# Performance work log

Hardware: AMD Instinct MI355X
Metric: run time of the kernel (lower is better)

Reference implementation:

```python
import jax, jax.numpy as jnp
import numpy as np

WS = 7
C = 384
NH = 12
HD = C // NH
HID = 4 * C


def layernorm(x, g, b, eps=1e-5):
    m = jnp.mean(x, axis=-1, keepdims=True)
    v = jnp.mean((x - m) ** 2, axis=-1, keepdims=True)
    return (x - m) * jax.lax.rsqrt(v + eps) * g + b


def setup_inputs() -> dict:
    key = jax.random.key(0)
    ks = jax.random.split(key, 12)
    s = 0.02
    return {
        "tokens": jax.random.normal(ks[0], (2, 8, 56 * 56, C), jnp.float32),
        "in_proj_w": jax.random.normal(ks[1], (3 * C, C), jnp.float32) * s,
        "in_proj_b": jnp.zeros((3 * C,), jnp.float32),
        "out_w": jax.random.normal(ks[2], (C, C), jnp.float32) * s,
        "out_b": jnp.zeros((C,), jnp.float32),
        "ln1_g": jnp.ones((C,), jnp.float32),
        "ln1_b": jnp.zeros((C,), jnp.float32),
        "w1": jax.random.normal(ks[3], (HID, C), jnp.float32) * s,
        "b1": jnp.zeros((HID,), jnp.float32),
        "w2": jax.random.normal(ks[4], (C, HID), jnp.float32) * s,
        "b2": jnp.zeros((C,), jnp.float32),
        "ln2_g": jnp.ones((C,), jnp.float32),
        "ln2_b": jnp.zeros((C,), jnp.float32),
        "h": 56,
        "w": 56,
    }


def _block(tokens, in_proj_w, in_proj_b, out_w, out_b, ln1_g, ln1_b, w1, b1, w2, b2, ln2_g, ln2_b, h, w):
    b, t, _, c = tokens.shape
    orig_h, orig_w = h, w
    x = tokens.reshape(b, t, h, w, c)
    pad_h = (-h) % WS
    pad_w = (-w) % WS
    if pad_h > 0 or pad_w > 0:
        x = jnp.pad(x, ((0, 0), (0, 0), (0, pad_h), (0, pad_w), (0, 0)))
        h, w = h + pad_h, w + pad_w
    nh, nw = h // WS, w // WS
    # window partition -> [N, 49, C]
    x = x.reshape(b, t, nh, WS, nw, WS, c).transpose(0, 1, 2, 4, 3, 5, 6)
    win = x.reshape(b * t * nh * nw, WS * WS, c)
    # MHA (torch nn.MultiheadAttention semantics)
    a = layernorm(win, ln1_g, ln1_b)
    qkv = a @ in_proj_w.T + in_proj_b  # [N, 49, 3C]
    q, k, v = jnp.split(qkv, 3, axis=-1)
    n, s, _ = q.shape
    q = q.reshape(n, s, NH, HD).transpose(0, 2, 1, 3)
    k = k.reshape(n, s, NH, HD).transpose(0, 2, 1, 3)
    v = v.reshape(n, s, NH, HD).transpose(0, 2, 1, 3)
    scores = jnp.einsum("nhqd,nhkd->nhqk", q, k) / jnp.sqrt(jnp.asarray(HD, q.dtype))
    p = jax.nn.softmax(scores, axis=-1)
    o = jnp.einsum("nhqk,nhkd->nhqd", p, v).transpose(0, 2, 1, 3).reshape(n, s, c)
    win = win + (o @ out_w.T + out_b)
    # MLP
    m = layernorm(win, ln2_g, ln2_b)
    m = jax.nn.gelu(m @ w1.T + b1, approximate=False) @ w2.T + b2
    win = win + m
    # window reverse
    x = win.reshape(b, t, nh, nw, WS, WS, c).transpose(0, 1, 2, 4, 3, 5, 6).reshape(b, t, h, w, c)
    x = x[:, :, :orig_h, :orig_w, :]
    return x.reshape(b, t, orig_h * orig_w, c)


def reference(tokens, in_proj_w, in_proj_b, out_w, out_b, ln1_g, ln1_b, w1, b1, w2, b2, ln2_g, ln2_b, h, w):
    return _block(tokens, in_proj_w, in_proj_b, out_w, out_b, ln1_g, ln1_b, w1, b1, w2, b2, ln2_g, ln2_b, h, w)
```

## Files before the change

kernel.cpp:

```cpp
#include <hip/hip_runtime.h>
#include <hip/hip_bf16.h>
#include <math.h>

using short8 = __attribute__((ext_vector_type(8))) short;
using f32x4  = __attribute__((ext_vector_type(4))) float;

#define MFMA_B16(A,B,C) __builtin_amdgcn_mfma_f32_16x16x32_bf16((A),(B),(C),0,0,0)

#define ALN_STR 392
#define Q2_OFF  38416
#define QK_STR  72
#define K2_OFF  45472
#define VT_OFF  52528
#define VT_STR  72
#define SC_OFF  61744
#define SC_STR  68
#define P_OFF   68408
#define P_STR   72
#define OH_OFF  75464
#define OH_STR  40
#define HID_OFF 38416
#define HID_STR 136
#define SMEM_BYTES 80896

__device__ __forceinline__ unsigned f2bf(float x) {
  unsigned u = __float_as_uint(x);
  return (u + 0x7fffu + ((u >> 16) & 1u)) >> 16;
}
__device__ __forceinline__ float bf2f(unsigned short b) {
  return __uint_as_float(((unsigned)b) << 16);
}

template<bool WBF>
__device__ __forceinline__ short8 loadW(const void* base, int tile, int K8, int kcb,
                                        int l, int row, int ldk, int k0) {
  if constexpr (WBF) {
    return *(const short8*)((const unsigned short*)base +
                            (((size_t)(tile * K8 + kcb)) << 7) + l * 8);
  } else {
    const float* p = (const float*)base + (size_t)row * ldk + k0;
    float4 x = *(const float4*)p;
    float4 y = *(const float4*)(p + 4);
    short8 r;
    r[0]=(short)f2bf(x.x); r[1]=(short)f2bf(x.y); r[2]=(short)f2bf(x.z); r[3]=(short)f2bf(x.w);
    r[4]=(short)f2bf(y.x); r[5]=(short)f2bf(y.y); r[6]=(short)f2bf(y.z); r[7]=(short)f2bf(y.w);
    return r;
  }
}

__global__ void cvt_pack(const float* __restrict__ src, unsigned short* __restrict__ dst,
                         int K, int n) {
  int K8 = K >> 3;
  int i = blockIdx.x * blockDim.x + threadIdx.x;
  if (i >= n) return;
  int e = i & 7;
  int idx = i >> 3;
  int r = idx & 15; idx >>= 4;
  int kc = idx % K8, ci = idx / K8;
  dst[i] = (unsigned short)f2bf(src[(size_t)(ci * 16 + r) * K + kc * 8 + e]);
}

template<bool WBF>
__global__ __launch_bounds__(512, 4)
void swin_mfma(const float* __restrict__ tokens,
               const void* __restrict__ ipw,  const float* __restrict__ ipb,
               const void* __restrict__ outw, const float* __restrict__ outb,
               const float* __restrict__ ln1g, const float* __restrict__ ln1b,
               const void* __restrict__ w1,   const float* __restrict__ b1,
               const void* __restrict__ w2,   const float* __restrict__ b2,
               const float* __restrict__ ln2g, const float* __restrict__ ln2b,
               float* __restrict__ out)
{
  extern __shared__ char smem[];
  unsigned short* aln = (unsigned short*)smem;
  unsigned short* q2  = (unsigned short*)(smem + Q2_OFF);
  unsigned short* k2  = (unsigned short*)(smem + K2_OFF);
  unsigned short* vT2 = (unsigned short*)(smem + VT_OFF);
  unsigned short* sc16= (unsigned short*)(smem + SC_OFF);
  unsigned short* P   = (unsigned short*)(smem + P_OFF);
  unsigned short* oh  = (unsigned short*)(smem + OH_OFF);
  unsigned short* hid = (unsigned short*)(smem + HID_OFF);

  const int tid = threadIdx.x;
  const int l  = tid & 63, wv = tid >> 6;
  const int cl = l & 15,  kg = l >> 4;
  const int wid = blockIdx.x;
  const int iw = wid & 7, ih = (wid >> 3) & 7, bt = wid >> 6;

  auto gidx = [&](int r, int c) -> size_t {
    int wi = r / 7, wj = r - wi * 7;
    return ((size_t)bt * 3136 + (size_t)((ih*7 + wi) * 56 + iw*7 + wj)) * 384 + c;
  };

  auto ln_pass = [&](const float* src, const float* gw, const float* gb) {
    int grp = tid >> 3, lj = tid & 7;
    if (grp < 49) {
      size_t base = gidx(grp, 0);
      float4 xv[12];
      float sx = 0.f, sxx = 0.f;
      #pragma unroll
      for (int k = 0; k < 12; ++k) {
        xv[k] = *(const float4*)&src[base + (lj + 8*k) * 4];
        sx  += xv[k].x + xv[k].y + xv[k].z + xv[k].w;
        sxx += xv[k].x*xv[k].x + xv[k].y*xv[k].y + xv[k].z*xv[k].z + xv[k].w*xv[k].w;
      }
      #pragma unroll
      for (int d = 1; d < 8; d <<= 1) { sx += __shfl_xor(sx, d, 8); sxx += __shfl_xor(sxx, d, 8); }
      float mean = sx * (1.f/384.f);
      float rs = rsqrtf(sxx * (1.f/384.f) - mean*mean + 1e-5f);
      unsigned short* arow = aln + grp * ALN_STR;
      #pragma unroll
      for (int k = 0; k < 12; ++k) {
        int c = (lj + 8*k) * 4;
        float4 gv = *(const float4*)&gw[c];
        float4 bv = *(const float4*)&gb[c];
        unsigned u0 = f2bf((xv[k].x-mean)*rs*gv.x + bv.x) | (f2bf((xv[k].y-mean)*rs*gv.y + bv.y) << 16);
        unsigned u1 = f2bf((xv[k].z-mean)*rs*gv.z + bv.z) | (f2bf((xv[k].w-mean)*rs*gv.w + bv.w) << 16);
        *(uint2*)&arow[c] = make_uint2(u0, u1);
      }
    }
  };

  for (int i = tid; i < (64*VT_STR)/2; i += 512) ((unsigned*)(smem + VT_OFF))[i] = 0u;
  for (int i = tid; i < (49*P_STR)/2;  i += 512) ((unsigned*)(smem + P_OFF))[i]  = 0u;
  ln_pass(tokens, ln1g, ln1b);
  __syncthreads();

  f32x4 opacc[3][4];
  #pragma unroll
  for (int a = 0; a < 3; ++a)
    #pragma unroll
    for (int b = 0; b < 4; ++b) opacc[a][b] = f32x4{0.f,0.f,0.f,0.f};

  const int ri0 = wv & 3, chalf = wv >> 2;
  const int arow0 = (cl + 16 * ri0) * ALN_STR;

  for (int pr = 0; pr < 6; ++pr) {
    #pragma unroll
    for (int half = 0; half < 2; ++half) {
      int cia[3], tilea[3], growa[3];
      #pragma unroll
      for (int j = 0; j < 3; ++j) {
        int ci = chalf + 2 * (half * 3 + j);
        int part = ci >> 2, wt = ci & 3;
        cia[j] = ci;
        tilea[j] = part * 24 + pr * 4 + wt;
        growa[j] = part * 384 + pr * 64 + wt * 16 + cl;
      }
      f32x4 d0{0,0,0,0}, d1{0,0,0,0}, d2{0,0,0,0};
      #pragma unroll
      for (int kt = 0; kt < 12; ++kt) {
        int k0 = kt * 32 + kg * 8;
        short8 a = *(const short8*)&aln[arow0 + k0];
        short8 b0 = loadW<WBF>(ipw, tilea[0], 48, kt*4, l, growa[0], 384, k0);
        short8 b1 = loadW<WBF>(ipw, tilea[1], 48, kt*4, l, growa[1], 384, k0);
        short8 b2 = loadW<WBF>(ipw, tilea[2], 48, kt*4, l, growa[2], 384, k0);
        d0 = MFMA_B16(a, b0, d0);
        d1 = MFMA_B16(a, b1, d1);
        d2 = MFMA_B16(a, b2, d2);
      }
      #pragma unroll
      for (int j = 0; j < 3; ++j) {
        f32x4 dd = (j == 0) ? d0 : (j == 1) ? d1 : d2;
        int part = cia[j] >> 2;
        int within = (cia[j] & 3) * 16 + cl;
        float bias = ipb[growa[j]];
        float scl = (part == 0) ? 0.17677669529663687f : 1.f;
        #pragma unroll
        for (int rg = 0; rg < 4; ++rg) {
          int row = kg * 4 + rg + 16 * ri0;
          if (row < 49) {
            unsigned short bv = (unsigned short)f2bf((dd[rg] + bias) * scl);
            if      (part == 0) q2[row * QK_STR + within] = bv;
            else if (part == 1) k2[row * QK_STR + within] = bv;
            else                vT2[within * VT_STR + row] = bv;
          }
        }
      }
    }
    __syncthreads();

    for (int hl = 0; hl < 2; ++hl) {
      int hh = 2 * pr + hl;
      short8 Bo0 = loadW<WBF>(outw, wv*3+0, 48, hh*4, l, (wv*3+0)*16+cl, 384, hh*32 + kg*8);
      short8 Bo1 = loadW<WBF>(outw, wv*3+1, 48, hh*4, l, (wv*3+1)*16+cl, 384, hh*32 + kg*8);
      short8 Bo2 = loadW<WBF>(outw, wv*3+2, 48, hh*4, l, (wv*3+2)*16+cl, 384, hh*32 + kg*8);

      #pragma unroll
      for (int tt = 0; tt < 2; ++tt) {
        int t = wv * 2 + tt, ri = t & 3, ci = t >> 2;
        short8 aq = *(const short8*)&q2[(cl + 16*ri) * QK_STR + hl*32 + kg*8];
        short8 bk = *(const short8*)&k2[(cl + 16*ci) * QK_STR + hl*32 + kg*8];
        f32x4 d{0,0,0,0};
        d = MFMA_B16(aq, bk, d);
        #pragma unroll
        for (int rg = 0; rg < 4; ++rg) {
          int row = kg * 4 + rg + 16 * ri;
          if (row < 49) sc16[row * SC_STR + ci*16 + cl] = (unsigned short)f2bf(d[rg]);
        }
      }
      __syncthreads();
      {
        int grp = tid >> 3, lj = tid & 7;
        if (grp < 49) {
          float vals[7]; float mx = -1e30f;
          #pragma unroll
          for (int k = 0; k < 7; ++k) {
            int j = lj + 8*k;
            float v = (j < 49) ? bf2f(sc16[grp * SC_STR + j]) : -1e30f;
            vals[k] = v; mx = fmaxf(mx, v);
          }
          #pragma unroll
          for (int d = 1; d < 8; d <<= 1) mx = fmaxf(mx, __shfl_xor(mx, d, 8));
          float sum = 0.f;
          #pragma unroll
          for (int k = 0; k < 7; ++k) { float e = __expf(vals[k] - mx); vals[k] = e; sum += e; }
          #pragma unroll
          for (int d = 1; d < 8; d <<= 1) sum += __shfl_xor(sum, d, 8);
          float inv = 1.f / sum;
          unsigned short* prow = &P[grp * P_STR];
          #pragma unroll
          for (int k = 0; k < 8; ++k) {
            int j = lj + 8*k;
            float pv = (k < 7 && j < 49) ? vals[k] * inv : 0.f;
            prow[j] = (unsigned short)f2bf(pv);
          }
        }
      }
      __syncthreads();
      {
        int ri = wv & 3, ci = wv >> 2;
        f32x4 d{0,0,0,0};
        #pragma unroll
        for (int kt = 0; kt < 2; ++kt) {
          short8 ap = *(const short8*)&P[(cl + 16*ri) * P_STR + kt*32 + kg*8];
          short8 bv = *(const short8*)&vT2[(hl*32 + ci*16 + cl) * VT_STR + kt*32 + kg*8];
          d = MFMA_B16(ap, bv, d);
        }
        #pragma unroll
        for (int rg = 0; rg < 4; ++rg) {
          int row = kg * 4 + rg + 16 * ri;
          if (row < 49) oh[row * OH_STR + ci*16 + cl] = (unsigned short)f2bf(d[rg]);
        }
      }
      __syncthreads();
      {
        short8 ao0 = *(const short8*)&oh[(cl     ) * OH_STR + kg*8];
        short8 ao1 = *(const short8*)&oh[(cl + 16) * OH_STR + kg*8];
        short8 ao2 = *(const short8*)&oh[(cl + 32) * OH_STR + kg*8];
        short8 ao3 = *(const short8*)&oh[(cl + 48) * OH_STR + kg*8];
        opacc[0][0] = MFMA_B16(ao0, Bo0, opacc[0][0]);
        opacc[0][1] = MFMA_B16(ao1, Bo0, opacc[0][1]);
        opacc[0][2] = MFMA_B16(ao2, Bo0, opacc[0][2]);
        opacc[0][3] = MFMA_B16(ao3, Bo0, opacc[0][3]);
        opacc[1][0] = MFMA_B16(ao0, Bo1, opacc[1][0]);
        opacc[1][1] = MFMA_B16(ao1, Bo1, opacc[1][1]);
        opacc[1][2] = MFMA_B16(ao2, Bo1, opacc[1][2]);
        opacc[1][3] = MFMA_B16(ao3, Bo1, opacc[1][3]);
        opacc[2][0] = MFMA_B16(ao0, Bo2, opacc[2][0]);
        opacc[2][1] = MFMA_B16(ao1, Bo2, opacc[2][1]);
        opacc[2][2] = MFMA_B16(ao2, Bo2, opacc[2][2]);
        opacc[2][3] = MFMA_B16(ao3, Bo2, opacc[2][3]);
      }
    }
  }

  #pragma unroll
  for (int cii = 0; cii < 3; ++cii) {
    int col = (wv*3 + cii) * 16 + cl;
    float ob = outb[col];
    #pragma unroll
    for (int ri = 0; ri < 4; ++ri) {
      #pragma unroll
      for (int rg = 0; rg < 4; ++rg) {
        int row = kg*4 + rg + 16*ri;
        if (row < 49) {
          size_t g = gidx(row, col);
          out[g] = tokens[g] + opacc[cii][ri][rg] + ob;
        }
      }
    }
  }
  __syncthreads();

  ln_pass(out, ln2g, ln2b);
  __syncthreads();

  f32x4 macc[3][4];
  #pragma unroll
  for (int a = 0; a < 3; ++a)
    #pragma unroll
    for (int b = 0; b < 4; ++b) macc[a][b] = f32x4{0.f,0.f,0.f,0.f};

  for (int cc = 0; cc < 12; ++cc) {
    {
      int tile = cc * 8 + wv;
      int n = cc * 128 + wv * 16 + cl;
      f32x4 e0{0,0,0,0}, e1{0,0,0,0}, e2{0,0,0,0}, e3{0,0,0,0};
      #pragma unroll
      for (int kt = 0; kt < 12; ++kt) {
        int k0 = kt * 32 + kg * 8;
        short8 bw = loadW<WBF>(w1, tile, 48, kt*4, l, n, 384, k0);
        short8 a0 = *(const short8*)&aln[(cl     ) * ALN_STR + k0];
        short8 a1 = *(const short8*)&aln[(cl + 16) * ALN_STR + k0];
        short8 a2 = *(const short8*)&aln[(cl + 32) * ALN_STR + k0];
        short8 a3 = *(const short8*)&aln[(cl + 48) * ALN_STR + k0];
        e0 = MFMA_B16(a0, bw, e0);
        e1 = MFMA_B16(a1, bw, e1);
        e2 = MFMA_B16(a2, bw, e2);
        e3 = MFMA_B16(a3, bw, e3);
      }
      float bb = b1[n];
      #pragma unroll
      for (int ri = 0; ri < 4; ++ri) {
        f32x4 ee = (ri == 0) ? e0 : (ri == 1) ? e1 : (ri == 2) ? e2 : e3;
        #pragma unroll
        for (int rg = 0; rg < 4; ++rg) {
          int row = kg*4 + rg + 16*ri;
          if (row < 49) {
            float x = ee[rg] + bb;
            float gl = 0.5f * x * (1.f + erff(x * 0.70710678118654752f));
            hid[row * HID_STR + wv*16 + cl] = (unsigned short)f2bf(gl);
          }
        }
      }
    }
    __syncthreads();
    #pragma unroll
    for (int kt = 0; kt < 4; ++kt) {
      int k0 = kt * 32 + kg * 8;
      short8 h0_ = *(const short8*)&hid[(cl     ) * HID_STR + k0];
      short8 h1_ = *(const short8*)&hid[(cl + 16) * HID_STR + k0];
      short8 h2_ = *(const short8*)&hid[(cl + 32) * HID_STR + k0];
      short8 h3_ = *(const short8*)&hid[(cl + 48) * HID_STR + k0];
      #pragma unroll
      for (int cii = 0; cii < 3; ++cii) {
        short8 bw = loadW<WBF>(w2, wv*3+cii, 192, cc*16 + kt*4, l,
                               (wv*3+cii)*16+cl, 1536, cc*128 + k0);
        macc[cii][0] = MFMA_B16(h0_, bw, macc[cii][0]);
        macc[cii][1] = MFMA_B16(h1_, bw, macc[cii][1]);
        macc[cii][2] = MFMA_B16(h2_, bw, macc[cii][2]);
        macc[cii][3] = MFMA_B16(h3_, bw, macc[cii][3]);
      }
    }
    __syncthreads();
  }

  #pragma unroll
  for (int cii = 0; cii < 3; ++cii) {
    int col = (wv*3 + cii) * 16 + cl;
    float bb2 = b2[col];
    #pragma unroll
    for (int ri = 0; ri < 4; ++ri) {
      #pragma unroll
      for (int rg = 0; rg < 4; ++rg) {
        int row = kg*4 + rg + 16*ri;
        if (row < 49) {
          size_t g = gidx(row, col);
          out[g] = out[g] + macc[cii][ri][rg] + bb2;
        }
      }
    }
  }
}

#define WS_IPW  0
#define WS_OUTW 442368
#define WS_W1   589824
#define WS_W2   1179648
#define WS_TOT  1769472

extern "C" void kernel_launch(void* const* d_in, const int* in_sizes, int n_in,
                              void* d_out, int out_size, void* d_ws, size_t ws_size,
                              hipStream_t stream) {
  (void)in_sizes; (void)n_in; (void)out_size;
  const float* tokens = (const float*)d_in[0];
  const float* ipw  = (const float*)d_in[1];
  const float* ipb  = (const float*)d_in[2];
  const float* outw = (const float*)d_in[3];
  const float* outb = (const float*)d_in[4];
  const float* ln1g = (const float*)d_in[5];
  const float* ln1b = (const float*)d_in[6];
  const float* w1   = (const float*)d_in[7];
  const float* b1   = (const float*)d_in[8];
  const float* w2   = (const float*)d_in[9];
  const float* b2   = (const float*)d_in[10];
  const float* ln2g = (const float*)d_in[11];
  const float* ln2b = (const float*)d_in[12];
  float* out = (float*)d_out;

  bool wbf = (ws_size >= (size_t)WS_TOT * 2);
  if (wbf) {
    unsigned short* wsp = (unsigned short*)d_ws;
    hipLaunchKernelGGL(cvt_pack, dim3((442368+511)/512), dim3(512), 0, stream, ipw,  wsp + WS_IPW,  384,  442368);
    hipLaunchKernelGGL(cvt_pack, dim3((147456+511)/512), dim3(512), 0, stream, outw, wsp + WS_OUTW, 384,  147456);
    hipLaunchKernelGGL(cvt_pack, dim3((589824+511)/512), dim3(512), 0, stream, w1,   wsp + WS_W1,   384,  589824);
    hipLaunchKernelGGL(cvt_pack, dim3((589824+511)/512), dim3(512), 0, stream, w2,   wsp + WS_W2,   1536, 589824);
    (void)hipFuncSetAttribute((const void*)swin_mfma<true>,
                              hipFuncAttributeMaxDynamicSharedMemorySize, SMEM_BYTES);
    hipLaunchKernelGGL((swin_mfma<true>), dim3(1024), dim3(512), SMEM_BYTES, stream,
                       tokens, (const void*)(wsp + WS_IPW), ipb,
                       (const void*)(wsp + WS_OUTW), outb, ln1g, ln1b,
                       (const void*)(wsp + WS_W1), b1, (const void*)(wsp + WS_W2), b2,
                       ln2g, ln2b, out);
  } else {
    (void)hipFuncSetAttribute((const void*)swin_mfma<false>,
                              hipFuncAttributeMaxDynamicSharedMemorySize, SMEM_BYTES);
    hipLaunchKernelGGL((swin_mfma<false>), dim3(1024), dim3(512), SMEM_BYTES, stream,
                       tokens, (const void*)ipw, ipb, (const void*)outw, outb, ln1g, ln1b,
                       (const void*)w1, b1, (const void*)w2, b2, ln2g, ln2b, out);
  }
}
```

Measured before the change: 499.6 us.

## Register-resident attention softmax and double-buffered hidden tiles to cut barriers

Attention scores are now computed per wave and kept in registers. Softmax uses cross-lane shuffles, and the P·V product takes its B fragment through lane shuffles instead of going through shared-memory score and probability buffers. Each pair of heads is handled in one pass, and the next QKV projection runs in the same sync interval as the out-projection. The MLP hidden buffer is double-buffered so that fc2 of one chunk overlaps fc1 of the next with one barrier per iteration. The aim is to remove many __syncthreads and shared-memory round trips. The cost is extra register pressure and shuffle traffic.

```diff
diff --git a/kernel.cpp b/kernel.cpp
--- a/kernel.cpp
+++ b/kernel.cpp
@@ -13,22 +13,16 @@
 #define K2_OFF  45472
 #define VT_OFF  52528
 #define VT_STR  72
-#define SC_OFF  61744
-#define SC_STR  68
-#define P_OFF   68408
-#define P_STR   72
-#define OH_OFF  75464
-#define OH_STR  40
-#define HID_OFF 38416
+#define OH_OFF  61744
+#define OH_STR  72
+#define HID0_OFF 38416
+#define HID1_OFF 55824
 #define HID_STR 136
 #define SMEM_BYTES 80896
 
 __device__ __forceinline__ unsigned f2bf(float x) {
   unsigned u = __float_as_uint(x);
   return (u + 0x7fffu + ((u >> 16) & 1u)) >> 16;
-}
-__device__ __forceinline__ float bf2f(unsigned short b) {
-  return __uint_as_float(((unsigned)b) << 16);
 }
 
 template<bool WBF>
@@ -72,14 +66,13 @@
                float* __restrict__ out)
 {
   extern __shared__ char smem[];
-  unsigned short* aln = (unsigned short*)smem;
-  unsigned short* q2  = (unsigned short*)(smem + Q2_OFF);
-  unsigned short* k2  = (unsigned short*)(smem + K2_OFF);
-  unsigned short* vT2 = (unsigned short*)(smem + VT_OFF);
-  unsigned short* sc16= (unsigned short*)(smem + SC_OFF);
-  unsigned short* P   = (unsigned short*)(smem + P_OFF);
-  unsigned short* oh  = (unsigned short*)(smem + OH_OFF);
-  unsigned short* hid = (unsigned short*)(smem + HID_OFF);
+  unsigned short* aln  = (unsigned short*)smem;
+  unsigned short* q2   = (unsigned short*)(smem + Q2_OFF);
+  unsigned short* k2   = (unsigned short*)(smem + K2_OFF);
+  unsigned short* vT2  = (unsigned short*)(smem + VT_OFF);
+  unsigned short* oh   = (unsigned short*)(smem + OH_OFF);
+  unsigned short* hid0 = (unsigned short*)(smem + HID0_OFF);
+  unsigned short* hid1 = (unsigned short*)(smem + HID1_OFF);
 
   const int tid = threadIdx.x;
   const int l  = tid & 63, wv = tid >> 6;
@@ -121,21 +114,10 @@
     }
   };
 
-  for (int i = tid; i < (64*VT_STR)/2; i += 512) ((unsigned*)(smem + VT_OFF))[i] = 0u;
-  for (int i = tid; i < (49*P_STR)/2;  i += 512) ((unsigned*)(smem + P_OFF))[i]  = 0u;
-  ln_pass(tokens, ln1g, ln1b);
-  __syncthreads();
-
-  f32x4 opacc[3][4];
-  #pragma unroll
-  for (int a = 0; a < 3; ++a)
-    #pragma unroll
-    for (int b = 0; b < 4; ++b) opacc[a][b] = f32x4{0.f,0.f,0.f,0.f};
-
   const int ri0 = wv & 3, chalf = wv >> 2;
   const int arow0 = (cl + 16 * ri0) * ALN_STR;
 
-  for (int pr = 0; pr < 6; ++pr) {
+  auto qkv = [&](int pr) {
     #pragma unroll
     for (int half = 0; half < 2; ++half) {
       int cia[3], tilea[3], growa[3];
@@ -178,91 +160,116 @@
         }
       }
     }
+  };
+
+  for (int i = tid; i < (64*VT_STR)/2; i += 512) ((unsigned*)(smem + VT_OFF))[i] = 0u;
+  ln_pass(tokens, ln1g, ln1b);
+  __syncthreads();
+
+  f32x4 opacc[3][4];
+  #pragma unroll
+  for (int a = 0; a < 3; ++a)
+    #pragma unroll
+    for (int b = 0; b < 4; ++b) opacc[a][b] = f32x4{0.f,0.f,0.f,0.f};
+
+  qkv(0);
+  __syncthreads();
+
+  const int hl = wv & 1, qci = wv >> 1;
+
+  for (int pr = 0; pr < 6; ++pr) {
+    {
+      short8 bq = *(const short8*)&q2[(16*qci + cl) * QK_STR + hl*32 + kg*8];
+      f32x4 dsc[4];
+      #pragma unroll
+      for (int kri = 0; kri < 4; ++kri) {
+        short8 ak = *(const short8*)&k2[(16*kri + cl) * QK_STR + hl*32 + kg*8];
+        f32x4 z{0.f,0.f,0.f,0.f};
+        dsc[kri] = MFMA_B16(ak, bq, z);
+      }
+      float ev[4][4];
+      float mx = -1e30f;
+      #pragma unroll
+      for (int kri = 0; kri < 4; ++kri)
+        #pragma unroll
+        for (int r = 0; r < 4; ++r) {
+          int kidx = 16*kri + 4*kg + r;
+          float v = (kidx < 49) ? dsc[kri][r] : -1e30f;
+          ev[kri][r] = v;
+          mx = fmaxf(mx, v);
+        }
+      mx = fmaxf(mx, __shfl_xor(mx, 16));
+      mx = fmaxf(mx, __shfl_xor(mx, 32));
+      float sum = 0.f;
+      #pragma unroll
+      for (int kri = 0; kri < 4; ++kri)
+        #pragma unroll
+        for (int r = 0; r < 4; ++r) {
+          float e = __expf(ev[kri][r] - mx);
+          ev[kri][r] = e; sum += e;
+        }
+      sum += __shfl_xor(sum, 16);
+      sum += __shfl_xor(sum, 32);
+      float inv = 1.f / sum;
+      unsigned pk[4][2];
+      #pragma unroll
+      for (int kri = 0; kri < 4; ++kri) {
+        pk[kri][0] = f2bf(ev[kri][0]*inv) | (f2bf(ev[kri][1]*inv) << 16);
+        pk[kri][1] = f2bf(ev[kri][2]*inv) | (f2bf(ev[kri][3]*inv) << 16);
+      }
+      f32x4 dot0{0.f,0.f,0.f,0.f}, dot1{0.f,0.f,0.f,0.f};
+      const int sA = cl + 32 * (kg & 1);
+      const bool hi = (kg >> 1) & 1;
+      #pragma unroll
+      for (int kt = 0; kt < 2; ++kt) {
+        unsigned x0 = (unsigned)__shfl((int)pk[2*kt][0],   sA);
+        unsigned x1 = (unsigned)__shfl((int)pk[2*kt][1],   sA);
+        unsigned x2 = (unsigned)__shfl((int)pk[2*kt][0],   sA + 16);
+        unsigned x3 = (unsigned)__shfl((int)pk[2*kt][1],   sA + 16);
+        unsigned y0 = (unsigned)__shfl((int)pk[2*kt+1][0], sA);
+        unsigned y1 = (unsigned)__shfl((int)pk[2*kt+1][1], sA);
+        unsigned y2 = (unsigned)__shfl((int)pk[2*kt+1][0], sA + 16);
+        unsigned y3 = (unsigned)__shfl((int)pk[2*kt+1][1], sA + 16);
+        uint4 bu = make_uint4(hi ? y0 : x0, hi ? y1 : x1, hi ? y2 : x2, hi ? y3 : x3);
+        short8 bfrag = *(short8*)&bu;
+        short8 a0 = *(const short8*)&vT2[(hl*32 +  0 + cl) * VT_STR + kt*32 + kg*8];
+        short8 a1 = *(const short8*)&vT2[(hl*32 + 16 + cl) * VT_STR + kt*32 + kg*8];
+        dot0 = MFMA_B16(a0, bfrag, dot0);
+        dot1 = MFMA_B16(a1, bfrag, dot1);
+      }
+      int q = 16*qci + cl;
+      if (q < 49) {
+        int base = q * OH_STR + hl*32 + kg*4;
+        *(unsigned*)&oh[base     ] = f2bf(dot0[0]) | (f2bf(dot0[1]) << 16);
+        *(unsigned*)&oh[base +  2] = f2bf(dot0[2]) | (f2bf(dot0[3]) << 16);
+        *(unsigned*)&oh[base + 16] = f2bf(dot1[0]) | (f2bf(dot1[1]) << 16);
+        *(unsigned*)&oh[base + 18] = f2bf(dot1[2]) | (f2bf(dot1[3]) << 16);
+      }
+    }
     __syncthreads();
 
-    for (int hl = 0; hl < 2; ++hl) {
-      int hh = 2 * pr + hl;
-      short8 Bo0 = loadW<WBF>(outw, wv*3+0, 48, hh*4, l, (wv*3+0)*16+cl, 384, hh*32 + kg*8);
-      short8 Bo1 = loadW<WBF>(outw, wv*3+1, 48, hh*4, l, (wv*3+1)*16+cl, 384, hh*32 + kg*8);
-      short8 Bo2 = loadW<WBF>(outw, wv*3+2, 48, hh*4, l, (wv*3+2)*16+cl, 384, hh*32 + kg*8);
-
-      #pragma unroll
-      for (int tt = 0; tt < 2; ++tt) {
-        int t = wv * 2 + tt, ri = t & 3, ci = t >> 2;
-        short8 aq = *(const short8*)&q2[(cl + 16*ri) * QK_STR + hl*32 + kg*8];
-        short8 bk = *(const short8*)&k2[(cl + 16*ci) * QK_STR + hl*32 + kg*8];
-        f32x4 d{0,0,0,0};
-        d = MFMA_B16(aq, bk, d);
+    {
+      short8 ao[4][2];
+      #pragma unroll
+      for (int ri = 0; ri < 4; ++ri)
         #pragma unroll
-        for (int rg = 0; rg < 4; ++rg) {
-          int row = kg * 4 + rg + 16 * ri;
-          if (row < 49) sc16[row * SC_STR + ci*16 + cl] = (unsigned short)f2bf(d[rg]);
-        }
-      }
-      __syncthreads();
-      {
-        int grp = tid >> 3, lj = tid & 7;
-        if (grp < 49) {
-          float vals[7]; float mx = -1e30f;
-          #pragma unroll
-          for (int k = 0; k < 7; ++k) {
-            int j = lj + 8*k;
-            float v = (j < 49) ? bf2f(sc16[grp * SC_STR + j]) : -1e30f;
-            vals[k] = v; mx = fmaxf(mx, v);
-          }
-          #pragma unroll
-          for (int d = 1; d < 8; d <<= 1) mx = fmaxf(mx, __shfl_xor(mx, d, 8));
-          float sum = 0.f;
-          #pragma unroll
-          for (int k = 0; k < 7; ++k) { float e = __expf(vals[k] - mx); vals[k] = e; sum += e; }
-          #pragma unroll
-          for (int d = 1; d < 8; d <<= 1) sum += __shfl_xor(sum, d, 8);
-          float inv = 1.f / sum;
-          unsigned short* prow = &P[grp * P_STR];
-          #pragma unroll
-          for (int k = 0; k < 8; ++k) {
-            int j = lj + 8*k;
-            float pv = (k < 7 && j < 49) ? vals[k] * inv : 0.f;
-            prow[j] = (unsigned short)f2bf(pv);
-          }
-        }
-      }
-      __syncthreads();
-      {
-        int ri = wv & 3, ci = wv >> 2;
-        f32x4 d{0,0,0,0};
+        for (int kt = 0; kt < 2; ++kt)
+          ao[ri][kt] = *(const short8*)&oh[(cl + 16*ri) * OH_STR + kt*32 + kg*8];
+      #pragma unroll
+      for (int cii = 0; cii < 3; ++cii) {
         #pragma unroll
         for (int kt = 0; kt < 2; ++kt) {
-          short8 ap = *(const short8*)&P[(cl + 16*ri) * P_STR + kt*32 + kg*8];
-          short8 bv = *(const short8*)&vT2[(hl*32 + ci*16 + cl) * VT_STR + kt*32 + kg*8];
-          d = MFMA_B16(ap, bv, d);
-        }
-        #pragma unroll
-        for (int rg = 0; rg < 4; ++rg) {
-          int row = kg * 4 + rg + 16 * ri;
-          if (row < 49) oh[row * OH_STR + ci*16 + cl] = (unsigned short)f2bf(d[rg]);
-        }
-      }
-      __syncthreads();
-      {
-        short8 ao0 = *(const short8*)&oh[(cl     ) * OH_STR + kg*8];
-        short8 ao1 = *(const short8*)&oh[(cl + 16) * OH_STR + kg*8];
-        short8 ao2 = *(const short8*)&oh[(cl + 32) * OH_STR + kg*8];
-        short8 ao3 = *(const short8*)&oh[(cl + 48) * OH_STR + kg*8];
-        opacc[0][0] = MFMA_B16(ao0, Bo0, opacc[0][0]);
-        opacc[0][1] = MFMA_B16(ao1, Bo0, opacc[0][1]);
-        opacc[0][2] = MFMA_B16(ao2, Bo0, opacc[0][2]);
-        opacc[0][3] = MFMA_B16(ao3, Bo0, opacc[0][3]);
-        opacc[1][0] = MFMA_B16(ao0, Bo1, opacc[1][0]);
-        opacc[1][1] = MFMA_B16(ao1, Bo1, opacc[1][1]);
-        opacc[1][2] = MFMA_B16(ao2, Bo1, opacc[1][2]);
-        opacc[1][3] = MFMA_B16(ao3, Bo1, opacc[1][3]);
-        opacc[2][0] = MFMA_B16(ao0, Bo2, opacc[2][0]);
-        opacc[2][1] = MFMA_B16(ao1, Bo2, opacc[2][1]);
-        opacc[2][2] = MFMA_B16(ao2, Bo2, opacc[2][2]);
-        opacc[2][3] = MFMA_B16(ao3, Bo2, opacc[2][3]);
-      }
-    }
+          short8 bw = loadW<WBF>(outw, wv*3 + cii, 48, pr*8 + kt*4, l,
+                                 (wv*3 + cii)*16 + cl, 384, pr*64 + kt*32 + kg*8);
+          opacc[cii][0] = MFMA_B16(ao[0][kt], bw, opacc[cii][0]);
+          opacc[cii][1] = MFMA_B16(ao[1][kt], bw, opacc[cii][1]);
+          opacc[cii][2] = MFMA_B16(ao[2][kt], bw, opacc[cii][2]);
+          opacc[cii][3] = MFMA_B16(ao[3][kt], bw, opacc[cii][3]);
+        }
+      }
+      if (pr < 5) qkv(pr + 1);
+    }
+    __syncthreads();
   }
 
   #pragma unroll
@@ -292,59 +299,66 @@
     #pragma unroll
     for (int b = 0; b < 4; ++b) macc[a][b] = f32x4{0.f,0.f,0.f,0.f};
 
-  for (int cc = 0; cc < 12; ++cc) {
-    {
-      int tile = cc * 8 + wv;
-      int n = cc * 128 + wv * 16 + cl;
-      f32x4 e0{0,0,0,0}, e1{0,0,0,0}, e2{0,0,0,0}, e3{0,0,0,0};
-      #pragma unroll
-      for (int kt = 0; kt < 12; ++kt) {
-        int k0 = kt * 32 + kg * 8;
-        short8 bw = loadW<WBF>(w1, tile, 48, kt*4, l, n, 384, k0);
-        short8 a0 = *(const short8*)&aln[(cl     ) * ALN_STR + k0];
-        short8 a1 = *(const short8*)&aln[(cl + 16) * ALN_STR + k0];
-        short8 a2 = *(const short8*)&aln[(cl + 32) * ALN_STR + k0];
-        short8 a3 = *(const short8*)&aln[(cl + 48) * ALN_STR + k0];
-        e0 = MFMA_B16(a0, bw, e0);
-        e1 = MFMA_B16(a1, bw, e1);
-        e2 = MFMA_B16(a2, bw, e2);
-        e3 = MFMA_B16(a3, bw, e3);
-      }
-      float bb = b1[n];
-      #pragma unroll
-      for (int ri = 0; ri < 4; ++ri) {
-        f32x4 ee = (ri == 0) ? e0 : (ri == 1) ? e1 : (ri == 2) ? e2 : e3;
-        #pragma unroll
-        for (int rg = 0; rg < 4; ++rg) {
-          int row = kg*4 + rg + 16*ri;
-          if (row < 49) {
-            float x = ee[rg] + bb;
-            float gl = 0.5f * x * (1.f + erff(x * 0.70710678118654752f));
-            hid[row * HID_STR + wv*16 + cl] = (unsigned short)f2bf(gl);
-          }
-        }
-      }
-    }
-    __syncthreads();
+  auto mlp1 = [&](int cc, unsigned short* hb) {
+    int tile = cc * 8 + wv;
+    int n = cc * 128 + wv * 16 + cl;
+    f32x4 e0{0,0,0,0}, e1{0,0,0,0}, e2{0,0,0,0}, e3{0,0,0,0};
+    #pragma unroll
+    for (int kt = 0; kt < 12; ++kt) {
+      int k0 = kt * 32 + kg * 8;
+      short8 bw = loadW<WBF>(w1, tile, 48, kt*4, l, n, 384, k0);
+      short8 a0 = *(const short8*)&aln[(cl     ) * ALN_STR + k0];
+      short8 a1 = *(const short8*)&aln[(cl + 16) * ALN_STR + k0];
+      short8 a2 = *(const short8*)&aln[(cl + 32) * ALN_STR + k0];
+      short8 a3 = *(const short8*)&aln[(cl + 48) * ALN_STR + k0];
+      e0 = MFMA_B16(a0, bw, e0);
+      e1 = MFMA_B16(a1, bw, e1);
+      e2 = MFMA_B16(a2, bw, e2);
+      e3 = MFMA_B16(a3, bw, e3);
+    }
+    float bb = b1[n];
+    #pragma unroll
+    for (int ri = 0; ri < 4; ++ri) {
+      f32x4 ee = (ri == 0) ? e0 : (ri == 1) ? e1 : (ri == 2) ? e2 : e3;
+      #pragma unroll
+      for (int rg = 0; rg < 4; ++rg) {
+        int row = kg*4 + rg + 16*ri;
+        if (row < 49) {
+          float x = ee[rg] + bb;
+          float gl = 0.5f * x * (1.f + erff(x * 0.70710678118654752f));
+          hb[row * HID_STR + wv*16 + cl] = (unsigned short)f2bf(gl);
+        }
+      }
+    }
+  };
+  auto mlp2 = [&](int cc, const unsigned short* hb) {
     #pragma unroll
     for (int kt = 0; kt < 4; ++kt) {
       int k0 = kt * 32 + kg * 8;
-      short8 h0_ = *(const short8*)&hid[(cl     ) * HID_STR + k0];
-      short8 h1_ = *(const short8*)&hid[(cl + 16) * HID_STR + k0];
-      short8 h2_ = *(const short8*)&hid[(cl + 32) * HID_STR + k0];
-      short8 h3_ = *(const short8*)&hid[(cl + 48) * HID_STR + k0];
+      short8 h0_ = *(const short8*)&hb[(cl     ) * HID_STR + k0];
+      short8 h1_ = *(const short8*)&hb[(cl + 16) * HID_STR + k0];
+      short8 h2_ = *(const short8*)&hb[(cl + 32) * HID_STR + k0];
+      short8 h3_ = *(const short8*)&hb[(cl + 48) * HID_STR + k0];
       #pragma unroll
       for (int cii = 0; cii < 3; ++cii) {
-        short8 bw = loadW<WBF>(w2, wv*3+cii, 192, cc*16 + kt*4, l,
-                               (wv*3+cii)*16+cl, 1536, cc*128 + k0);
+        short8 bw = loadW<WBF>(w2, wv*3 + cii, 192, cc*16 + kt*4, l,
+                               (wv*3 + cii)*16 + cl, 1536, cc*128 + k0);
         macc[cii][0] = MFMA_B16(h0_, bw, macc[cii][0]);
         macc[cii][1] = MFMA_B16(h1_, bw, macc[cii][1]);
         macc[cii][2] = MFMA_B16(h2_, bw, macc[cii][2]);
         macc[cii][3] = MFMA_B16(h3_, bw, macc[cii][3]);
       }
     }
+  };
+
+  mlp1(0, hid0);
+  __syncthreads();
+  for (int cc = 1; cc < 12; ++cc) {
+    mlp2(cc - 1, ((cc - 1) & 1) ? hid1 : hid0);
+    mlp1(cc, (cc & 1) ? hid1 : hid0);
     __syncthreads();
   }
+  mlp2(11, hid1);
 
   #pragma unroll
   for (int cii = 0; cii < 3; ++cii) {
```

Result: faster. 475.2 us (-4.9%).
